# Performance work log

Hardware: AMD Instinct MI355X
Metric: run time of the kernel (lower is better)

The kernel has to match this reference:

```python
import jax, jax.numpy as jnp
import numpy as np

S, D, H, F = 8192, 2048, 2048, 8192
C_GATE = 8.0
EPS = 1e-6


def _rmsnorm(x, w, b):
    # eqx.nn.RMSNorm: x / sqrt(mean(x^2) + eps) * w + b, per row
    inv = jax.lax.rsqrt(jnp.mean(x * x, axis=-1, keepdims=True) + EPS)
    return x * inv * w + b


def _rglru(x, W_in, b_in, W_a, b_a, W_g, b_g, lam, W_out, b_out):
    # Real-Gated LRU (Griffin). x: [S, D] -> [S, D], hidden state size H.
    xh = x @ W_in.T + b_in                      # [S, H]
    r = jax.nn.sigmoid(x @ W_a.T + b_a)         # recurrence gate [S, H]
    g = jax.nn.sigmoid(x @ W_g.T + b_g)         # input gate      [S, H]
    log_a = C_GATE * r * jax.nn.log_sigmoid(lam)  # log a_t, a = sigmoid(lam)^(c*r)
    a = jnp.exp(log_a)                          # [S, H], in (0,1)
    b = jnp.sqrt(1.0 - jnp.exp(2.0 * log_a)) * (g * xh)

    def combine(e1, e2):
        a1, b1 = e1
        a2, b2 = e2
        return (a1 * a2, a2 * b1 + b2)

    _, h = jax.lax.associative_scan(combine, (a, b), axis=0)  # h_t = a_t h_{t-1} + b_t
    return h @ W_out.T + b_out                  # [S, D]


def _ffn(x, w1, b1, w2, b2):
    return jax.nn.gelu(x @ w1.T + b1) @ w2.T + b2


def setup_inputs() -> dict:
    key = jax.random.key(0)
    ks = jax.random.split(key, 16)
    s = 0.02  # weight init scale
    return {
        "x": jax.random.normal(ks[0], (S, D), jnp.float32),
        "W_in": jax.random.normal(ks[1], (H, D), jnp.float32) * s,
        "b_in": jnp.zeros((H,), jnp.float32),
        "W_a": jax.random.normal(ks[2], (H, D), jnp.float32) * s,
        "b_a": jnp.zeros((H,), jnp.float32),
        "W_g": jax.random.normal(ks[3], (H, D), jnp.float32) * s,
        "b_g": jnp.zeros((H,), jnp.float32),
        "lam": jax.random.normal(ks[4], (H,), jnp.float32),
        "W_out": jax.random.normal(ks[5], (D, H), jnp.float32) * s,
        "b_out": jnp.zeros((D,), jnp.float32),
        "ffn_w1": jax.random.normal(ks[6], (F, D), jnp.float32) * s,
        "ffn_b1": jnp.zeros((F,), jnp.float32),
        "ffn_w2": jax.random.normal(ks[7], (D, F), jnp.float32) * s,
        "ffn_b2": jnp.zeros((D,), jnp.float32),
        "act1_w": jax.random.normal(ks[8], (1, D), jnp.float32) * s,
        "act1_b": jnp.zeros((1,), jnp.float32),
        "act2_w": jax.random.normal(ks[9], (1, D), jnp.float32) * s,
        "act2_b": jnp.zeros((1,), jnp.float32),
        "norm1_w": jnp.ones((D,), jnp.float32),
        "norm1_b": jnp.zeros((D,), jnp.float32),
        "norm2_w": jnp.ones((D,), jnp.float32),
        "norm2_b": jnp.zeros((D,), jnp.float32),
        "u1": jax.random.uniform(ks[10], (S, 1), jnp.float32),
        "u2": jax.random.uniform(ks[11], (S, 1), jnp.float32),
    }


def reference(x, W_in, b_in, W_a, b_a, W_g, b_g, lam, W_out, b_out,
              ffn_w1, ffn_b1, ffn_w2, ffn_b2,
              act1_w, act1_b, act2_w, act2_b,
              norm1_w, norm1_b, norm2_w, norm2_b, u1, u2):
    # --- RG-LRU branch (dropout p=0 -> identity) ---
    residual = _rglru(x, W_in, b_in, W_a, b_a, W_g, b_g, lam, W_out, b_out)
    act_prob = jax.nn.sigmoid(residual @ act1_w.T + act1_b)  # [S, 1]
    act = u1 < act_prob                                      # stochastic gate
    residual = jnp.where(act, residual, 0.0)
    x = _rmsnorm(x + residual, norm1_w, norm1_b)
    # --- FFN branch ---
    residual = _ffn(x, ffn_w1, ffn_b1, ffn_w2, ffn_b2)
    act_prob = jax.nn.sigmoid(residual @ act2_w.T + act2_b)
    act = u2 < act_prob
    residual = jnp.where(act, residual, 0.0)
    x = _rmsnorm(x + residual, norm2_w, norm2_b)
    return x
```

## Files before the change

### kernel.cpp

```cpp
#include <hip/hip_runtime.h>

#define LDSW 40
#define SCAN_P 128
#define SCAN_L 64

typedef short short8 __attribute__((ext_vector_type(8)));
typedef float floatx4 __attribute__((ext_vector_type(4)));
typedef unsigned short u16;

__device__ __forceinline__ u16 bf16_rne(float v) {
    unsigned int u = __float_as_uint(v);
    u = u + 0x7fffu + ((u >> 16) & 1u);
    return (u16)(u >> 16);
}
__device__ __forceinline__ float bf16_to_f(u16 h) {
    return __uint_as_float(((unsigned int)h) << 16);
}
__device__ __forceinline__ float sigm(float x) { return 1.f / (1.f + expf(-x)); }
__device__ __forceinline__ float logsig(float x) {
    const float l = log1pf(expf(-fabsf(x)));
    return x >= 0.f ? -l : x - l;
}

__device__ __forceinline__ void cvt8(const float* p, short8& h8, short8& l8) {
    const float4 a = *(const float4*)p;
    const float4 b = *(const float4*)(p + 4);
    const float v[8] = {a.x, a.y, a.z, a.w, b.x, b.y, b.z, b.w};
#pragma unroll
    for (int j = 0; j < 8; ++j) {
        const u16 hh = bf16_rne(v[j]);
        h8[j] = (short)hh;
        l8[j] = (short)bf16_rne(v[j] - bf16_to_f(hh));
    }
}
__device__ __forceinline__ void cvt8h(const float* p, short8& h8) {
    const float4 a = *(const float4*)p;
    const float4 b = *(const float4*)(p + 4);
    const float v[8] = {a.x, a.y, a.z, a.w, b.x, b.y, b.z, b.w};
#pragma unroll
    for (int j = 0; j < 8; ++j) h8[j] = (short)bf16_rne(v[j]);
}

__device__ __forceinline__ void gld16(const u16* g, u16* l) {
    __builtin_amdgcn_global_load_lds(
        (const __attribute__((address_space(1))) void*)g,
        (__attribute__((address_space(3))) void*)l, 16, 0, 0);
}

template <int AFMT, int NPROD, int EPI, int ACC, int ST>
__global__ __launch_bounds__(256, 2) void gemm_f32(
    const float* __restrict__ Af, const u16* __restrict__ Au,
    const float* __restrict__ Bf, const float* __restrict__ bias,
    float* C, u16* Chi, u16* Clo, const float* Q,
    long ldA, long ldB, long ldC, int K)
{
    __shared__ __align__(16) u16 sAh[128 * LDSW];
    __shared__ __align__(16) u16 sBh[128 * LDSW];
    __shared__ __align__(16) u16 sAl[NPROD == 3 ? 128 * LDSW : 8];
    __shared__ __align__(16) u16 sBl[NPROD == 3 ? 128 * LDSW : 8];

    const int tid  = threadIdx.x;
    const int lane = tid & 63;
    const int wid  = tid >> 6;
    const int wm   = (wid >> 1) << 6;
    const int wn   = (wid & 1) << 6;
    const int m16  = lane & 15;
    const int kq   = lane >> 4;
    const int koff = kq << 3;
    const long bM  = (long)blockIdx.y << 7;
    const long bN  = (long)blockIdx.x << 7;
    const int sr   = tid >> 2;
    const int sc   = (tid & 3) << 3;

    floatx4 acc[4][4] = {};

#pragma unroll 1
    for (int k0 = 0; k0 < K; k0 += 32) {
        __syncthreads();
#pragma unroll
        for (int i = 0; i < 2; ++i) {
            const int r  = sr + (i << 6);
            const int ls = r * LDSW + sc;
            if constexpr (AFMT == 0) {
                if constexpr (NPROD == 3) {
                    short8 h8, l8;
                    cvt8(Af + (bM + r) * ldA + k0 + sc, h8, l8);
                    *(short8*)&sAh[ls] = h8;
                    *(short8*)&sAl[ls] = l8;
                } else {
                    short8 h8;
                    cvt8h(Af + (bM + r) * ldA + k0 + sc, h8);
                    *(short8*)&sAh[ls] = h8;
                }
            } else {
                *(short8*)&sAh[ls] = *(const short8*)(Au + (bM + r) * ldA + k0 + sc);
            }
            if constexpr (NPROD == 3) {
                short8 h8, l8;
                cvt8(Bf + (bN + r) * ldB + k0 + sc, h8, l8);
                *(short8*)&sBh[ls] = h8;
                *(short8*)&sBl[ls] = l8;
            } else {
                short8 h8;
                cvt8h(Bf + (bN + r) * ldB + k0 + sc, h8);
                *(short8*)&sBh[ls] = h8;
            }
        }
        __syncthreads();

        short8 ah[4], bh[4];
#pragma unroll
        for (int t = 0; t < 4; ++t) {
            ah[t] = *(const short8*)&sAh[(wm + t * 16 + m16) * LDSW + koff];
            bh[t] = *(const short8*)&sBh[(wn + t * 16 + m16) * LDSW + koff];
        }
#pragma unroll
        for (int mi = 0; mi < 4; ++mi)
#pragma unroll
            for (int ni = 0; ni < 4; ++ni)
                acc[mi][ni] = __builtin_amdgcn_mfma_f32_16x16x32_bf16(ah[mi], bh[ni], acc[mi][ni], 0, 0, 0);

        if constexpr (NPROD == 3) {
            short8 al[4], bl[4];
#pragma unroll
            for (int t = 0; t < 4; ++t) {
                al[t] = *(const short8*)&sAl[(wm + t * 16 + m16) * LDSW + koff];
                bl[t] = *(const short8*)&sBl[(wn + t * 16 + m16) * LDSW + koff];
            }
#pragma unroll
            for (int mi = 0; mi < 4; ++mi)
#pragma unroll
                for (int ni = 0; ni < 4; ++ni)
                    acc[mi][ni] = __builtin_amdgcn_mfma_f32_16x16x32_bf16(ah[mi], bl[ni], acc[mi][ni], 0, 0, 0);
#pragma unroll
            for (int mi = 0; mi < 4; ++mi)
#pragma unroll
                for (int ni = 0; ni < 4; ++ni)
                    acc[mi][ni] = __builtin_amdgcn_mfma_f32_16x16x32_bf16(al[mi], bh[ni], acc[mi][ni], 0, 0, 0);
        }
    }

    float bv[4];
#pragma unroll
    for (int ni = 0; ni < 4; ++ni) bv[ni] = bias ? bias[bN + wn + ni * 16 + m16] : 0.f;

#pragma unroll
    for (int mi = 0; mi < 4; ++mi) {
#pragma unroll
        for (int ni = 0; ni < 4; ++ni) {
#pragma unroll
            for (int r = 0; r < 4; ++r) {
                const long grow = bM + wm + mi * 16 + (kq << 2) + r;
                const long gcol = bN + wn + ni * 16 + m16;
                const long idx  = grow * ldC + gcol;
                float v = acc[mi][ni][r] + bv[ni];
                if constexpr (ACC) v += C[idx];
                if constexpr (EPI == 1) v *= Q[idx];
                if constexpr (EPI == 2)
                    v = 0.5f * v * (1.f + tanhf(0.7978845608028654f * (v + 0.044715f * v * v * v)));
                if constexpr (ST == 1) {
                    const u16 h = bf16_rne(v);
                    Chi[idx] = h;
                    Clo[idx] = bf16_rne(v - bf16_to_f(h));
                } else {
                    C[idx] = v;
                }
            }
        }
    }
}

template <int NPROD, int BFMT, int EPI, int ACC, int ST, int DOT>
__global__ __launch_bounds__(256, 2) void gemm_sp(
    const u16* __restrict__ Ah, const u16* __restrict__ Al,
    const u16* __restrict__ Bh, const u16* __restrict__ Bl,
    const float* __restrict__ Bf, const float* __restrict__ bias,
    float* C, u16* Chi, const float* Q,
    const float* __restrict__ vvec, float* dacc,
    long ldA, long ldB, long ldC, int K)
{
    __shared__ __align__(16) u16 sAh[128 * 32];
    __shared__ __align__(16) u16 sBh[128 * 32];
    __shared__ __align__(16) u16 sAl[NPROD == 3 ? 128 * 32 : 8];
    __shared__ __align__(16) u16 sBl[NPROD == 3 ? 128 * 32 : 8];

    const int tid  = threadIdx.x;
    const int lane = tid & 63;
    const int wid  = tid >> 6;
    const int wm   = (wid >> 1) << 6;
    const int wn   = (wid & 1) << 6;
    const int m16  = lane & 15;
    const int kq   = lane >> 4;
    const long bM  = (long)blockIdx.y << 7;
    const long bN  = (long)blockIdx.x << 7;

    const int  drow = (wid << 5) + (lane >> 2);
    const int  qsrc = (((lane & 3) ^ ((lane >> 3) & 3)) << 3);
    const long a0   = (bM + drow) * ldA + qsrc;
    const long a1   = a0 + 16 * ldA;
    const long b0   = (bN + drow) * ldB + qsrc;
    const long b1   = b0 + 16 * ldB;
    u16* const lA0  = &sAh[(wid << 5) << 5];
    u16* const lA1  = lA0 + 512;
    u16* const lB0  = &sBh[(wid << 5) << 5];
    u16* const lB1  = lB0 + 512;
    u16* const lAl0 = &sAl[NPROD == 3 ? ((wid << 5) << 5) : 0];
    u16* const lAl1 = lAl0 + (NPROD == 3 ? 512 : 0);
    u16* const lBl0 = &sBl[NPROD == 3 ? ((wid << 5) << 5) : 0];
    u16* const lBl1 = lBl0 + (NPROD == 3 ? 512 : 0);

    const int sr  = tid >> 2;
    const int sc  = (tid & 3) << 3;
    const int wch = (((tid & 3) ^ ((sr >> 1) & 3)) << 3);

    const int kr = ((kq ^ ((m16 >> 1) & 3)) << 3);

    floatx4 acc[4][4] = {};

#pragma unroll 1
    for (int k0 = 0; k0 < K; k0 += 32) {
        __syncthreads();
        gld16(Ah + a0 + k0, lA0);
        gld16(Ah + a1 + k0, lA1);
        if constexpr (NPROD == 3) {
            gld16(Al + a0 + k0, lAl0);
            gld16(Al + a1 + k0, lAl1);
        }
        if constexpr (BFMT == 1) {
            gld16(Bh + b0 + k0, lB0);
            gld16(Bh + b1 + k0, lB1);
            if constexpr (NPROD == 3) {
                gld16(Bl + b0 + k0, lBl0);
                gld16(Bl + b1 + k0, lBl1);
            }
        } else {
#pragma unroll
            for (int i = 0; i < 2; ++i) {
                const int r = sr + (i << 6);
                short8 h8, l8;
                cvt8(Bf + (bN + r) * ldB + k0 + sc, h8, l8);
                *(short8*)&sBh[(r << 5) + wch] = h8;
                *(short8*)&sBl[(r << 5) + wch] = l8;
            }
        }
        __syncthreads();

        short8 ah[4], bh[4];
#pragma unroll
        for (int t = 0; t < 4; ++t) {
            ah[t] = *(const short8*)&sAh[((wm + t * 16 + m16) << 5) + kr];
            bh[t] = *(const short8*)&sBh[((wn + t * 16 + m16) << 5) + kr];
        }
#pragma unroll
        for (int mi = 0; mi < 4; ++mi)
#pragma unroll
            for (int ni = 0; ni < 4; ++ni)
                acc[mi][ni] = __builtin_amdgcn_mfma_f32_16x16x32_bf16(ah[mi], bh[ni], acc[mi][ni], 0, 0, 0);

        if constexpr (NPROD == 3) {
            short8 al[4], bl[4];
#pragma unroll
            for (int t = 0; t < 4; ++t) {
                al[t] = *(const short8*)&sAl[((wm + t * 16 + m16) << 5) + kr];
                bl[t] = *(const short8*)&sBl[((wn + t * 16 + m16) << 5) + kr];
            }
#pragma unroll
            for (int mi = 0; mi < 4; ++mi)
#pragma unroll
                for (int ni = 0; ni < 4; ++ni)
                    acc[mi][ni] = __builtin_amdgcn_mfma_f32_16x16x32_bf16(ah[mi], bl[ni], acc[mi][ni], 0, 0, 0);
#pragma unroll
            for (int mi = 0; mi < 4; ++mi)
#pragma unroll
                for (int ni = 0; ni < 4; ++ni)
                    acc[mi][ni] = __builtin_amdgcn_mfma_f32_16x16x32_bf16(al[mi], bh[ni], acc[mi][ni], 0, 0, 0);
        }
    }

    float bv[4];
#pragma unroll
    for (int ni = 0; ni < 4; ++ni) bv[ni] = bias ? bias[bN + wn + ni * 16 + m16] : 0.f;
    float vv[4] = {}, ls[4] = {};
    if constexpr (EPI == 3 || DOT == 1) {
#pragma unroll
        for (int ni = 0; ni < 4; ++ni) {
            vv[ni] = vvec[bN + wn + ni * 16 + m16];
            if constexpr (EPI == 3) ls[ni] = logsig(vv[ni]);
        }
    }
    float ds[4][4] = {};

#pragma unroll
    for (int mi = 0; mi < 4; ++mi) {
#pragma unroll
        for (int ni = 0; ni < 4; ++ni) {
#pragma unroll
            for (int r = 0; r < 4; ++r) {
                const long grow = bM + wm + mi * 16 + (kq << 2) + r;
                const long gcol = bN + wn + ni * 16 + m16;
                const long idx  = grow * ldC + gcol;
                float v = acc[mi][ni][r] + bv[ni];
                if constexpr (EPI == 1) v *= Q[idx];
                if constexpr (EPI == 2)
                    v = 0.5f * v * (1.f + tanhf(0.7978845608028654f * (v + 0.044715f * v * v * v)));
                if constexpr (EPI == 3) v = expf(8.f * sigm(v) * ls[ni]);
                if constexpr (EPI == 4) {
                    const float a = Q[idx];
                    v = sqrtf(fmaxf(1.f - a * a, 0.f)) * sigm(v);
                }
                if constexpr (ACC) v += C[idx];
                if constexpr (DOT) ds[mi][r] += v * vv[ni];
                if constexpr (ST == 1) Chi[idx] = bf16_rne(v);
                else C[idx] = v;
            }
        }
    }

    if constexpr (DOT) {
#pragma unroll
        for (int mi = 0; mi < 4; ++mi)
#pragma unroll
            for (int r = 0; r < 4; ++r) {
                float s = ds[mi][r];
                s += __shfl_xor(s, 1);
                s += __shfl_xor(s, 2);
                s += __shfl_xor(s, 4);
                s += __shfl_xor(s, 8);
                if (m16 == 0)
                    atomicAdd(&dacc[bM + wm + mi * 16 + (kq << 2) + r], s);
            }
    }
}

template <int HASLO>
__global__ __launch_bounds__(256) void split_kernel(
    const float* __restrict__ src, long lds,
    u16* __restrict__ hi, u16* __restrict__ lo, long ldd)
{
    const long r = blockIdx.x;
    const int  c = threadIdx.x << 3;
    const float* p = src + r * lds + c;
    const float4 a = *(const float4*)p;
    const float4 b = *(const float4*)(p + 4);
    const float v[8] = {a.x, a.y, a.z, a.w, b.x, b.y, b.z, b.w};
    short8 h8, l8;
#pragma unroll
    for (int j = 0; j < 8; ++j) {
        const u16 hh = bf16_rne(v[j]);
        h8[j] = (short)hh;
        if constexpr (HASLO) l8[j] = (short)bf16_rne(v[j] - bf16_to_f(hh));
    }
    *(short8*)&hi[r * ldd + c] = h8;
    if constexpr (HASLO) *(short8*)&lo[r * ldd + c] = l8;
}

__global__ __launch_bounds__(256) void zb2init_kernel(
    float* __restrict__ zb2, const float* __restrict__ zc2)
{
    zb2[blockIdx.x * 256 + threadIdx.x] = zc2[0];
}

__global__ __launch_bounds__(256) void aq_kernel(
    float* za, float* zg, const float* __restrict__ lam)
{
    const long i = ((long)blockIdx.x * 256 + threadIdx.x) * 4;
    const int  c = (int)(i & 2047);
    const float4 zav = *(const float4*)(za + i);
    const float4 zgv = *(const float4*)(zg + i);
    const float4 lmv = *(const float4*)(lam + c);
    float4 av, qv;
    const float zaa[4] = {zav.x, zav.y, zav.z, zav.w};
    const float zga[4] = {zgv.x, zgv.y, zgv.z, zgv.w};
    const float lma[4] = {lmv.x, lmv.y, lmv.z, lmv.w};
    float aa[4], qa[4];
#pragma unroll
    for (int j = 0; j < 4; ++j) {
        const float r  = sigm(zaa[j]);
        const float g  = sigm(zga[j]);
        const float la = 8.f * r * logsig(lma[j]);
        aa[j] = expf(la);
        qa[j] = sqrtf(fmaxf(1.f - expf(2.f * la), 0.f)) * g;
    }
    av.x = aa[0]; av.y = aa[1]; av.z = aa[2]; av.w = aa[3];
    qv.x = qa[0]; qv.y = qa[1]; qv.z = qa[2]; qv.w = qa[3];
    *(float4*)(za + i) = av;
    *(float4*)(zg + i) = qv;
}

__global__ __launch_bounds__(256) void scan_partial(
    const float* __restrict__ A, const float* __restrict__ B,
    float* __restrict__ Aagg, float* __restrict__ Bagg)
{
    const int c = blockIdx.x * 256 + threadIdx.x;
    const int p = blockIdx.y;
    const long base = (long)p * SCAN_L * 2048 + c;
    float Ar = 1.f, Br = 0.f;
    for (int t = 0; t < SCAN_L; ++t) {
        const float at = A[base + (long)t * 2048];
        const float bt = B[base + (long)t * 2048];
        Ar *= at;
        Br = Br * at + bt;
    }
    Aagg[p * 2048 + c] = Ar;
    Bagg[p * 2048 + c] = Br;
}

__global__ __launch_bounds__(256) void scan_combine(
    const float* __restrict__ Aagg, const float* __restrict__ Bagg,
    float* __restrict__ Hini)
{
    const int c = blockIdx.x * 256 + threadIdx.x;
    float h = 0.f;
    for (int p = 0; p < SCAN_P; ++p) {
        Hini[p * 2048 + c] = h;
        h = Aagg[p * 2048 + c] * h + Bagg[p * 2048 + c];
    }
}

__global__ __launch_bounds__(256) void scan_final(
    float* A, const float* __restrict__ B, const float* __restrict__ Hini)
{
    const int c = blockIdx.x * 256 + threadIdx.x;
    const int p = blockIdx.y;
    const long base = (long)p * SCAN_L * 2048 + c;
    float h = Hini[p * 2048 + c];
    for (int t = 0; t < SCAN_L; ++t) {
        const long idx = base + (long)t * 2048;
        h = A[idx] * h + B[idx];
        A[idx] = h;
    }
}

__global__ __launch_bounds__(256) void vpart_kernel(
    const float* __restrict__ W, const float* __restrict__ w,
    float* __restrict__ part, long ldW, int dchunk)
{
    const int j  = blockIdx.x * 256 + threadIdx.x;
    const int d0 = blockIdx.y * dchunk;
    float s = 0.f;
    for (int d = 0; d < dchunk; ++d) s += W[(long)(d0 + d) * ldW + j] * w[d0 + d];
    part[(long)blockIdx.y * ldW + j] = s;
}

__global__ __launch_bounds__(256) void vreduce_kernel(
    const float* __restrict__ part, float* __restrict__ v, long ldW, int nch)
{
    const int j = blockIdx.x * 256 + threadIdx.x;
    float s = 0.f;
    for (int c = 0; c < nch; ++c) s += part[(long)c * ldW + j];
    v[j] = s;
}

__global__ __launch_bounds__(256) void dotc_kernel(
    const float* __restrict__ a, const float* __restrict__ b,
    const float* __restrict__ bias1, float* __restrict__ out)
{
    __shared__ float red[4];
    const int tid = threadIdx.x, lane = tid & 63, wid = tid >> 6;
    float s = 0.f;
    for (int d = tid; d < 2048; d += 256) s += a[d] * b[d];
#pragma unroll
    for (int off = 32; off > 0; off >>= 1) s += __shfl_down(s, off);
    if (lane == 0) red[wid] = s;
    __syncthreads();
    if (tid == 0) out[0] = red[0] + red[1] + red[2] + red[3] + bias1[0];
}

template <int INIT>
__global__ __launch_bounds__(256) void zacc_kernel(
    const u16* __restrict__ uHi, const u16* __restrict__ uLo,
    const float* __restrict__ v2s, const float* __restrict__ zc,
    float* __restrict__ zb, int L)
{
    __shared__ float red[4];
    const int tid = threadIdx.x, lane = tid & 63, wid = tid >> 6;
    const long s = blockIdx.x;
    const long base = s * (long)L;
    float dot = 0.f;
    for (int f = tid; f < L; f += 256)
        dot += (bf16_to_f(uHi[base + f]) + bf16_to_f(uLo[base + f])) * v2s[f];
#pragma unroll
    for (int off = 32; off > 0; off >>= 1) dot += __shfl_down(dot, off);
    if (lane == 0) red[wid] = dot;
    __syncthreads();
    if (tid == 0) {
        const float t = red[0] + red[1] + red[2] + red[3];
        zb[s] = INIT ? (zc[0] + t) : (zb[s] + t);
    }
}

__global__ __launch_bounds__(256) void gate1_kernel(
    const float* __restrict__ x, float* res1x1,
    const float* __restrict__ h,
    const float* __restrict__ v1, const float* __restrict__ zc1,
    const float* __restrict__ u1,
    const float* __restrict__ nw, const float* __restrict__ nb)
{
    __shared__ float red[4];
    const int tid = threadIdx.x, lane = tid & 63, wid = tid >> 6;
    const long s = blockIdx.x;
    const long base = s * 2048;

    float dot = 0.f;
#pragma unroll
    for (int k = 0; k < 8; ++k) {
        const int d = tid + (k << 8);
        dot += h[base + d] * v1[d];
    }
#pragma unroll
    for (int off = 32; off > 0; off >>= 1) dot += __shfl_down(dot, off);
    if (lane == 0) red[wid] = dot;
    __syncthreads();
    const float z = red[0] + red[1] + red[2] + red[3] + zc1[0];
    __syncthreads();

    const float g = (u1[s] < sigm(z)) ? 1.f : 0.f;

    float yv[8];
    float ss = 0.f;
#pragma unroll
    for (int k = 0; k < 8; ++k) {
        const int d = tid + (k << 8);
        const float y = x[base + d] + g * res1x1[base + d];
        yv[k] = y;
        ss += y * y;
    }
#pragma unroll
    for (int off = 32; off > 0; off >>= 1) ss += __shfl_down(ss, off);
    if (lane == 0) red[wid] = ss;
    __syncthreads();
    const float inv = rsqrtf((red[0] + red[1] + red[2] + red[3]) * (1.f / 2048.f) + 1e-6f);

#pragma unroll
    for (int k = 0; k < 8; ++k) {
        const int d = tid + (k << 8);
        res1x1[base + d] = yv[k] * inv * nw[d] + nb[d];
    }
}

__global__ __launch_bounds__(256) void gate1s_kernel(
    const float* __restrict__ x, float* res1x1,
    const float* __restrict__ h,
    const float* __restrict__ v1, const float* __restrict__ zc1,
    const float* __restrict__ u1,
    const float* __restrict__ nw, const float* __restrict__ nb)
{
    __shared__ float red[4];
    const int tid = threadIdx.x, lane = tid & 63, wid = tid >> 6;
    const long s = blockIdx.x;
    const long base = s * 2048;

    float dot = 0.f;
#pragma unroll
    for (int k = 0; k < 8; ++k) {
        const int d = tid + (k << 8);
        dot += h[base + d] * v1[d];
    }
#pragma unroll
    for (int off = 32; off > 0; off >>= 1) dot += __shfl_down(dot, off);
    if (lane == 0) red[wid] = dot;
    __syncthreads();
    const float z = red[0] + red[1] + red[2] + red[3] + zc1[0];
    __syncthreads();

    const float g = (u1[s] < sigm(z)) ? 1.f : 0.f;

    float yv[8];
    float ss = 0.f;
#pragma unroll
    for (int k = 0; k < 8; ++k) {
        const int d = tid + (k << 8);
        const float y = x[base + d] + g * res1x1[base + d];
        yv[k] = y;
        ss += y * y;
    }
#pragma unroll
    for (int off = 32; off > 0; off >>= 1) ss += __shfl_down(ss, off);
    if (lane == 0) red[wid] = ss;
    __syncthreads();
    const float inv = rsqrtf((red[0] + red[1] + red[2] + red[3]) * (1.f / 2048.f) + 1e-6f);

    u16* xs = (u16*)res1x1;
    const long sb = s * 4096;
#pragma unroll
    for (int k = 0; k < 8; ++k) {
        const int d = tid + (k << 8);
        const float o = yv[k] * inv * nw[d] + nb[d];
        const u16 hh = bf16_rne(o);
        xs[sb + d] = hh;
        xs[sb + 2048 + d] = bf16_rne(o - bf16_to_f(hh));
    }
}

__global__ __launch_bounds__(256) void gate2_kernel(
    float* x1out, const float* __restrict__ res2,
    const float* __restrict__ zb2, const float* __restrict__ u2,
    const float* __restrict__ nw, const float* __restrict__ nb)
{
    __shared__ float red[4];
    const int tid = threadIdx.x, lane = tid & 63, wid = tid >> 6;
    const long s = blockIdx.x;
    const long base = s * 2048;

    const float g = (u2[s] < sigm(zb2[s])) ? 1.f : 0.f;

    float yv[8];
    float ss = 0.f;
#pragma unroll
    for (int k = 0; k < 8; ++k) {
        const int d = tid + (k << 8);
        const float y = x1out[base + d] + g * res2[base + d];
        yv[k] = y;
        ss += y * y;
    }
#pragma unroll
    for (int off = 32; off > 0; off >>= 1) ss += __shfl_down(ss, off);
    if (lane == 0) red[wid] = ss;
    __syncthreads();
    const float inv = rsqrtf((red[0] + red[1] + red[2] + red[3]) * (1.f / 2048.f) + 1e-6f);

#pragma unroll
    for (int k = 0; k < 8; ++k) {
        const int d = tid + (k << 8);
        x1out[base + d] = yv[k] * inv * nw[d] + nb[d];
    }
}

__global__ __launch_bounds__(256) void gate2s_kernel(
    float* x1out, const float* __restrict__ res2,
    const float* __restrict__ zb2, const float* __restrict__ u2,
    const float* __restrict__ nw, const float* __restrict__ nb)
{
    __shared__ float red[4];
    const int tid = threadIdx.x, lane = tid & 63, wid = tid >> 6;
    const long s = blockIdx.x;
    const long base = s * 2048;
    const u16* xs = (const u16*)x1out;
    const long sb = s * 4096;

    const float g = (u2[s] < sigm(zb2[s])) ? 1.f : 0.f;

    float yv[8];
    float ss = 0.f;
#pragma unroll
    for (int k = 0; k < 8; ++k) {
        const int d = tid + (k << 8);
        const float x1 = bf16_to_f(xs[sb + d]) + bf16_to_f(xs[sb + 2048 + d]);
        const float y = x1 + g * res2[base + d];
        yv[k] = y;
        ss += y * y;
    }
#pragma unroll
    for (int off = 32; off > 0; off >>= 1) ss += __shfl_down(ss, off);
    if (lane == 0) red[wid] = ss;
    __syncthreads();
    const float inv = rsqrtf((red[0] + red[1] + red[2] + red[3]) * (1.f / 2048.f) + 1e-6f);

#pragma unroll
    for (int k = 0; k < 8; ++k) {
        const int d = tid + (k << 8);
        x1out[base + d] = yv[k] * inv * nw[d] + nb[d];
    }
}

extern "C" void kernel_launch(void* const* d_in, const int* in_sizes, int n_in,
                              void* d_out, int out_size, void* d_ws, size_t ws_size,
                              hipStream_t stream)
{
    const float* x     = (const float*)d_in[0];
    const float* W_in  = (const float*)d_in[1];
    const float* b_in  = (const float*)d_in[2];
    const float* W_a   = (const float*)d_in[3];
    const float* b_a   = (const float*)d_in[4];
    const float* W_g   = (const float*)d_in[5];
    const float* b_g   = (const float*)d_in[6];
    const float* lam   = (const float*)d_in[7];
    const float* W_out = (const float*)d_in[8];
    const float* b_out = (const float*)d_in[9];
    const float* w1    = (const float*)d_in[10];
    const float* fb1   = (const float*)d_in[11];
    const float* w2    = (const float*)d_in[12];
    const float* fb2   = (const float*)d_in[13];
    const float* a1w   = (const float*)d_in[14];
    const float* a1b   = (const float*)d_in[15];
    const float* a2w   = (const float*)d_in[16];
    const float* a2b   = (const float*)d_in[17];
    const float* n1w   = (const float*)d_in[18];
    const float* n1b   = (const float*)d_in[19];
    const float* n2w   = (const float*)d_in[20];
    const float* n2b   = (const float*)d_in[21];
    const float* u1    = (const float*)d_in[22];
    const float* u2    = (const float*)d_in[23];
    (void)in_sizes; (void)n_in; (void)out_size;

    float* dob = (float*)d_out;

    char* ws = (char*)d_ws;
    size_t o = 0;
    auto take = [&](size_t bytes) -> char* {
        char* p = ws + o;
        o += (bytes + 255) & ~(size_t)255;
        return p;
    };

    float* Aagg = (float*)take((size_t)SCAN_P * 2048 * 4);
    float* Bagg = (float*)take((size_t)SCAN_P * 2048 * 4);
    float* Hini = (float*)take((size_t)SCAN_P * 2048 * 4);
    float* v1   = (float*)take(2048 * 4);
    float* v2   = (float*)take(8192 * 4);
    float* vp   = (float*)take(16 * 8192 * 4);
    float* zc1  = (float*)take(256);
    float* zc2  = (float*)take(256);
    float* zb2  = (float*)take(8192 * 4);

    float* slabA = (float*)take(64ull << 20);
    const bool pathA = ws_size >= o + (64ull << 20);
    float* slabB = nullptr;
    float* res2b = nullptr;
    if (pathA) slabB = (float*)take(64ull << 20);
    else       res2b = (float*)take(16ull << 20);
    if (o > ws_size) return;

    const dim3 blk(256);

    vpart_kernel<<<dim3(8, 16), blk, 0, stream>>>(W_out, a1w, vp, 2048, 128);
    vreduce_kernel<<<8, blk, 0, stream>>>(vp, v1, 2048, 16);
    vpart_kernel<<<dim3(32, 16), blk, 0, stream>>>(w2, a2w, vp, 8192, 128);
    vreduce_kernel<<<32, blk, 0, stream>>>(vp, v2, 8192, 16);
    dotc_kernel<<<1, blk, 0, stream>>>(b_out, a1w, a1b, zc1);
    dotc_kernel<<<1, blk, 0, stream>>>(fb2, a2w, a2b, zc2);

    if (pathA) {
        u16* const xh = (u16*)slabA;
        u16* const xl = xh + (1u << 24);
        split_kernel<1><<<8192, blk, 0, stream>>>(x, 2048, xh, xl, 2048);

        gemm_sp<3, 0, 3, 0, 0, 0><<<dim3(16, 64), blk, 0, stream>>>(
            xh, xl, nullptr, nullptr, W_a, b_a, slabB, nullptr, nullptr, lam, nullptr,
            2048, 2048, 2048, 2048);
        gemm_sp<3, 0, 4, 0, 0, 0><<<dim3(16, 64), blk, 0, stream>>>(
            xh, xl, nullptr, nullptr, W_g, b_g, dob, nullptr, slabB, nullptr, nullptr,
            2048, 2048, 2048, 2048);
        gemm_sp<3, 0, 1, 0, 0, 0><<<dim3(16, 64), blk, 0, stream>>>(
            xh, xl, nullptr, nullptr, W_in, b_in, dob, nullptr, dob, nullptr, nullptr,
            2048, 2048, 2048, 2048);

        scan_partial<<<dim3(8, SCAN_P), blk, 0, stream>>>(slabB, dob, Aagg, Bagg);
        scan_combine<<<8, blk, 0, stream>>>(Aagg, Bagg, Hini);
        scan_final<<<dim3(8, SCAN_P), blk, 0, stream>>>(slabB, dob, Hini);

        u16* const hH  = (u16*)slabA;
        u16* const woH = hH + (1u << 24);
        split_kernel<0><<<8192, blk, 0, stream>>>(slabB, 2048, hH, nullptr, 2048);
        split_kernel<0><<<2048, blk, 0, stream>>>(W_out, 2048, woH, nullptr, 2048);
        gemm_sp<1, 1, 0, 0, 0, 0><<<dim3(16, 64), blk, 0, stream>>>(
            hH, nullptr, woH, nullptr, nullptr, b_out, dob, nullptr, nullptr, nullptr, nullptr,
            2048, 2048, 2048, 2048);

        gate1s_kernel<<<8192, blk, 0, stream>>>(x, dob, slabB, v1, zc1, u1, n1w, n1b);

        zb2init_kernel<<<32, blk, 0, stream>>>(zb2, zc2);

        u16* const uH  = (u16*)slabA;
        u16* const w1H = uH + (1u << 24);
        u16* const w1L = w1H + (1u << 22);
        u16* const w2H = w1H + (1u << 23);
        u16* const x1h = (u16*)dob;
        for (int c = 0; c < 4; ++c) {
            const long f0 = (long)c << 11;
            split_kernel<1><<<2048, blk, 0, stream>>>(w1 + f0 * 2048, 2048, w1H, w1L, 2048);
            split_kernel<0><<<2048, blk, 0, stream>>>(w2 + f0, 8192, w2H, nullptr, 2048);
            gemm_sp<3, 1, 2, 0, 1, 1><<<dim3(16, 64), blk, 0, stream>>>(
                x1h, x1h + 2048, w1H, w1L, nullptr, fb1 + f0, nullptr, uH, nullptr,
                v2 + f0, zb2, 4096, 2048, 2048, 2048);
            if (c == 0)
                gemm_sp<1, 1, 0, 0, 0, 0><<<dim3(16, 64), blk, 0, stream>>>(
                    uH, nullptr, w2H, nullptr, nullptr, fb2, slabB, nullptr, nullptr,
                    nullptr, nullptr, 2048, 2048, 2048, 2048);
            else
                gemm_sp<1, 1, 0, 1, 0, 0><<<dim3(16, 64), blk, 0, stream>>>(
                    uH, nullptr, w2H, nullptr, nullptr, nullptr, slabB, nullptr, nullptr,
                    nullptr, nullptr, 2048, 2048, 2048, 2048);
        }
        gate2s_kernel<<<8192, blk, 0, stream>>>(dob, slabB, zb2, u2, n2w, n2b);
    } else {
        u16* uHi = (u16*)slabA;
        u16* uLo = uHi + (1u << 24);

        gemm_f32<0, 3, 0, 0, 0><<<dim3(16, 64), blk, 0, stream>>>(
            x, nullptr, W_a, b_a, slabA, nullptr, nullptr, nullptr, 2048, 2048, 2048, 2048);
        gemm_f32<0, 3, 0, 0, 0><<<dim3(16, 64), blk, 0, stream>>>(
            x, nullptr, W_g, b_g, dob, nullptr, nullptr, nullptr, 2048, 2048, 2048, 2048);
        aq_kernel<<<16384, blk, 0, stream>>>(slabA, dob, lam);
        gemm_f32<0, 3, 1, 0, 0><<<dim3(16, 64), blk, 0, stream>>>(
            x, nullptr, W_in, b_in, dob, nullptr, nullptr, dob, 2048, 2048, 2048, 2048);
        scan_partial<<<dim3(8, SCAN_P), blk, 0, stream>>>(slabA, dob, Aagg, Bagg);
        scan_combine<<<8, blk, 0, stream>>>(Aagg, Bagg, Hini);
        scan_final<<<dim3(8, SCAN_P), blk, 0, stream>>>(slabA, dob, Hini);
        gemm_f32<0, 1, 0, 0, 0><<<dim3(16, 64), blk, 0, stream>>>(
            slabA, nullptr, W_out, b_out, dob, nullptr, nullptr, nullptr, 2048, 2048, 2048, 2048);
        gate1_kernel<<<8192, blk, 0, stream>>>(x, dob, slabA, v1, zc1, u1, n1w, n1b);
        for (int rb = 0; rb < 4; ++rb) {
            const long roff = (long)rb * 2048;
            gemm_f32<0, 3, 2, 0, 1><<<dim3(64, 16), blk, 0, stream>>>(
                dob + roff * 2048, nullptr, w1, fb1,
                nullptr, uHi, uLo, nullptr, 2048, 2048, 8192, 2048);
            zacc_kernel<1><<<2048, blk, 0, stream>>>(uHi, uLo, v2, zc2, zb2 + roff, 8192);
            gemm_f32<1, 1, 0, 0, 0><<<dim3(16, 16), blk, 0, stream>>>(
                nullptr, uHi, w2, fb2, res2b, nullptr, nullptr, nullptr,
                8192, 8192, 2048, 8192);
            gate2_kernel<<<2048, blk, 0, stream>>>(
                dob + roff * 2048, res2b, zb2 + roff, u2 + roff, n2w, n2b);
        }
    }
}
```

Baseline: 2.686 ms.

## Add 256x256-tile 512-thread bf16 MFMA GEMM and fuse h bf16 split into scan

Introduces gemm8, a 512-thread kernel computing 256x256 output tiles. It double-buffers global-to-LDS loads with explicit vmcnt waits, uses XOR-swizzled LDS reads, and raises wave priority around the MFMA blocks. This kernel replaces gemm_sp for the W_out projection and the FFN w1 and w2 GEMMs. Separately, scan_final now writes the bf16 copy of h directly, which removes one split_kernel pass over the 8192x2048 hidden state. Larger tiles cut global traffic per FLOP, but they raise register and LDS pressure and halve the number of blocks, which could hurt occupancy and load balance.

```diff
diff --git a/kernel.cpp b/kernel.cpp
--- a/kernel.cpp
+++ b/kernel.cpp
@@ -46,6 +46,12 @@
         (const __attribute__((address_space(1))) void*)g,
         (__attribute__((address_space(3))) void*)l, 16, 0, 0);
 }
+
+__device__ __forceinline__ void vmwait8() { asm volatile("s_waitcnt vmcnt(8)" ::: "memory"); }
+__device__ __forceinline__ void vmwait4() { asm volatile("s_waitcnt vmcnt(4)" ::: "memory"); }
+__device__ __forceinline__ void vmwait0() { asm volatile("s_waitcnt vmcnt(0)" ::: "memory"); }
+__device__ __forceinline__ void lgwait0() { asm volatile("s_waitcnt lgkmcnt(0)" ::: "memory"); }
+__device__ __forceinline__ void barr()    { asm volatile("s_barrier" ::: "memory"); }
 
 template <int AFMT, int NPROD, int EPI, int ACC, int ST>
 __global__ __launch_bounds__(256, 2) void gemm_f32(
@@ -332,6 +338,195 @@
     }
 }
 
+template <int NPROD, int EPI, int ACC, int ST, int DOT>
+__global__ __launch_bounds__(512, 2) void gemm8(
+    const u16* __restrict__ Ah, const u16* __restrict__ Al,
+    const u16* __restrict__ Bh, const u16* __restrict__ Bl,
+    const float* __restrict__ bias,
+    float* C, u16* Chi,
+    const float* __restrict__ vvec, float* dacc,
+    long ldA, long ldB, long ldC, int K)
+{
+    constexpr int NPL = (NPROD == 3) ? 4 : 2;
+    __shared__ __align__(16) u16 lds[2][NPL][8192];
+
+    const int tid  = threadIdx.x;
+    const int lane = tid & 63;
+    const int wid  = tid >> 6;
+    const int wr   = wid >> 2;
+    const int wc   = wid & 3;
+    const int m16  = lane & 15;
+    const int kq   = lane >> 4;
+    const long bM  = (long)blockIdx.y << 8;
+    const long bN  = (long)blockIdx.x << 8;
+
+    const int  drow = (wid << 5) + (lane >> 2);
+    const int  qsrc = (((lane & 3) ^ ((lane >> 3) & 3)) << 3);
+    const u16* gA0  = Ah + (bM + drow) * ldA + qsrc;
+    const u16* gA1  = gA0 + (ldA << 4);
+    const u16* gB0  = Bh + (bN + drow) * ldB + qsrc;
+    const u16* gB1  = gB0 + (ldB << 4);
+    const u16* gAl0 = (NPROD == 3 ? Al : Ah) + (bM + drow) * ldA + qsrc;
+    const u16* gAl1 = gAl0 + (ldA << 4);
+    const u16* gBl0 = (NPROD == 3 ? Bl : Bh) + (bN + drow) * ldB + qsrc;
+    const u16* gBl1 = gBl0 + (ldB << 4);
+
+    const int lwb = wid << 10;
+    const int kr  = ((kq ^ ((m16 >> 1) & 3)) << 3);
+
+    const int NT = K >> 5;
+
+    auto stage = [&](int buf, int t) {
+        const long k0 = (long)t << 5;
+        gld16(gA0 + k0, &lds[buf][0][lwb]);
+        gld16(gA1 + k0, &lds[buf][0][lwb + 512]);
+        gld16(gB0 + k0, &lds[buf][1][lwb]);
+        gld16(gB1 + k0, &lds[buf][1][lwb + 512]);
+        if constexpr (NPROD == 3) {
+            gld16(gAl0 + k0, &lds[buf][2][lwb]);
+            gld16(gAl1 + k0, &lds[buf][2][lwb + 512]);
+            gld16(gBl0 + k0, &lds[buf][3][lwb]);
+            gld16(gBl1 + k0, &lds[buf][3][lwb + 512]);
+        }
+    };
+
+    floatx4 acc[8][4] = {};
+    short8 bh[4], bl[4];
+
+    stage(0, 0);
+    stage(1, 1);
+    if constexpr (NPROD == 3) vmwait8(); else vmwait4();
+    barr();
+
+    const int arow = (wr << 7) + m16;
+    const int brow = (wc << 6) + m16;
+
+#pragma unroll 1
+    for (int t = 0; t < NT; ++t) {
+        const int p = t & 1;
+#pragma unroll
+        for (int q = 0; q < 4; ++q) {
+            const int r0 = arow + (q << 5);
+            const int r1 = r0 + 16;
+            short8 ah0 = *(const short8*)&lds[p][0][(r0 << 5) + kr];
+            short8 ah1 = *(const short8*)&lds[p][0][(r1 << 5) + kr];
+            short8 al0 = {}, al1 = {};
+            if constexpr (NPROD == 3) {
+                al0 = *(const short8*)&lds[p][2][(r0 << 5) + kr];
+                al1 = *(const short8*)&lds[p][2][(r1 << 5) + kr];
+            }
+            if (q == 0) {
+#pragma unroll
+                for (int ni = 0; ni < 4; ++ni) {
+                    const int rb = (brow + (ni << 4)) << 5;
+                    bh[ni] = *(const short8*)&lds[p][1][rb + kr];
+                    if constexpr (NPROD == 3)
+                        bl[ni] = *(const short8*)&lds[p][3][rb + kr];
+                }
+            }
+            if (q < 3) {
+                lgwait0();
+                __builtin_amdgcn_sched_barrier(0);
+                __builtin_amdgcn_s_setprio(1);
+#pragma unroll
+                for (int ni = 0; ni < 4; ++ni) {
+                    acc[2 * q][ni]     = __builtin_amdgcn_mfma_f32_16x16x32_bf16(ah0, bh[ni], acc[2 * q][ni], 0, 0, 0);
+                    acc[2 * q + 1][ni] = __builtin_amdgcn_mfma_f32_16x16x32_bf16(ah1, bh[ni], acc[2 * q + 1][ni], 0, 0, 0);
+                }
+                if constexpr (NPROD == 3) {
+#pragma unroll
+                    for (int ni = 0; ni < 4; ++ni) {
+                        acc[2 * q][ni]     = __builtin_amdgcn_mfma_f32_16x16x32_bf16(ah0, bl[ni], acc[2 * q][ni], 0, 0, 0);
+                        acc[2 * q + 1][ni] = __builtin_amdgcn_mfma_f32_16x16x32_bf16(ah1, bl[ni], acc[2 * q + 1][ni], 0, 0, 0);
+                    }
+#pragma unroll
+                    for (int ni = 0; ni < 4; ++ni) {
+                        acc[2 * q][ni]     = __builtin_amdgcn_mfma_f32_16x16x32_bf16(al0, bh[ni], acc[2 * q][ni], 0, 0, 0);
+                        acc[2 * q + 1][ni] = __builtin_amdgcn_mfma_f32_16x16x32_bf16(al1, bh[ni], acc[2 * q + 1][ni], 0, 0, 0);
+                    }
+                }
+                __builtin_amdgcn_s_setprio(0);
+                barr();
+            } else {
+                lgwait0();
+                barr();
+                const bool pf = (t + 2 < NT);
+                if (pf) stage(p, t + 2);
+                __builtin_amdgcn_s_setprio(1);
+#pragma unroll
+                for (int ni = 0; ni < 4; ++ni) {
+                    acc[6][ni] = __builtin_amdgcn_mfma_f32_16x16x32_bf16(ah0, bh[ni], acc[6][ni], 0, 0, 0);
+                    acc[7][ni] = __builtin_amdgcn_mfma_f32_16x16x32_bf16(ah1, bh[ni], acc[7][ni], 0, 0, 0);
+                }
+                if constexpr (NPROD == 3) {
+#pragma unroll
+                    for (int ni = 0; ni < 4; ++ni) {
+                        acc[6][ni] = __builtin_amdgcn_mfma_f32_16x16x32_bf16(ah0, bl[ni], acc[6][ni], 0, 0, 0);
+                        acc[7][ni] = __builtin_amdgcn_mfma_f32_16x16x32_bf16(ah1, bl[ni], acc[7][ni], 0, 0, 0);
+                    }
+#pragma unroll
+                    for (int ni = 0; ni < 4; ++ni) {
+                        acc[6][ni] = __builtin_amdgcn_mfma_f32_16x16x32_bf16(al0, bh[ni], acc[6][ni], 0, 0, 0);
+                        acc[7][ni] = __builtin_amdgcn_mfma_f32_16x16x32_bf16(al1, bh[ni], acc[7][ni], 0, 0, 0);
+                    }
+                }
+                __builtin_amdgcn_s_setprio(0);
+                if (pf) {
+                    if constexpr (NPROD == 3) vmwait8(); else vmwait4();
+                } else {
+                    vmwait0();
+                }
+                barr();
+            }
+        }
+    }
+
+    float bv[4];
+#pragma unroll
+    for (int ni = 0; ni < 4; ++ni) bv[ni] = bias ? bias[bN + (wc << 6) + (ni << 4) + m16] : 0.f;
+    float vv[4] = {};
+    if constexpr (DOT) {
+#pragma unroll
+        for (int ni = 0; ni < 4; ++ni) vv[ni] = vvec[bN + (wc << 6) + (ni << 4) + m16];
+    }
+    float ds[8][4] = {};
+
+#pragma unroll
+    for (int mi = 0; mi < 8; ++mi) {
+#pragma unroll
+        for (int ni = 0; ni < 4; ++ni) {
+#pragma unroll
+            for (int r = 0; r < 4; ++r) {
+                const long grow = bM + (wr << 7) + (mi << 4) + (kq << 2) + r;
+                const long gcol = bN + (wc << 6) + (ni << 4) + m16;
+                const long idx  = grow * ldC + gcol;
+                float v = acc[mi][ni][r] + bv[ni];
+                if constexpr (EPI == 2)
+                    v = 0.5f * v * (1.f + tanhf(0.7978845608028654f * (v + 0.044715f * v * v * v)));
+                if constexpr (ACC) v += C[idx];
+                if constexpr (DOT) ds[mi][r] += v * vv[ni];
+                if constexpr (ST == 1) Chi[idx] = bf16_rne(v);
+                else C[idx] = v;
+            }
+        }
+    }
+
+    if constexpr (DOT) {
+#pragma unroll
+        for (int mi = 0; mi < 8; ++mi)
+#pragma unroll
+            for (int r = 0; r < 4; ++r) {
+                float s = ds[mi][r];
+                s += __shfl_xor(s, 1);
+                s += __shfl_xor(s, 2);
+                s += __shfl_xor(s, 4);
+                s += __shfl_xor(s, 8);
+                if (m16 == 0)
+                    atomicAdd(&dacc[bM + (wr << 7) + (mi << 4) + (kq << 2) + r], s);
+            }
+    }
+}
+
 template <int HASLO>
 __global__ __launch_bounds__(256) void split_kernel(
     const float* __restrict__ src, long lds,
@@ -418,7 +613,8 @@
 }
 
 __global__ __launch_bounds__(256) void scan_final(
-    float* A, const float* __restrict__ B, const float* __restrict__ Hini)
+    float* A, const float* __restrict__ B, const float* __restrict__ Hini,
+    u16* __restrict__ Hhi)
 {
     const int c = blockIdx.x * 256 + threadIdx.x;
     const int p = blockIdx.y;
@@ -428,6 +624,7 @@
         const long idx = base + (long)t * 2048;
         h = A[idx] * h + B[idx];
         A[idx] = h;
+        if (Hhi) Hhi[idx] = bf16_rne(h);
     }
 }
 
@@ -745,16 +942,15 @@
             xh, xl, nullptr, nullptr, W_in, b_in, dob, nullptr, dob, nullptr, nullptr,
             2048, 2048, 2048, 2048);
 
+        u16* const hH = (u16*)slabA;
         scan_partial<<<dim3(8, SCAN_P), blk, 0, stream>>>(slabB, dob, Aagg, Bagg);
         scan_combine<<<8, blk, 0, stream>>>(Aagg, Bagg, Hini);
-        scan_final<<<dim3(8, SCAN_P), blk, 0, stream>>>(slabB, dob, Hini);
-
-        u16* const hH  = (u16*)slabA;
+        scan_final<<<dim3(8, SCAN_P), blk, 0, stream>>>(slabB, dob, Hini, hH);
+
         u16* const woH = hH + (1u << 24);
-        split_kernel<0><<<8192, blk, 0, stream>>>(slabB, 2048, hH, nullptr, 2048);
         split_kernel<0><<<2048, blk, 0, stream>>>(W_out, 2048, woH, nullptr, 2048);
-        gemm_sp<1, 1, 0, 0, 0, 0><<<dim3(16, 64), blk, 0, stream>>>(
-            hH, nullptr, woH, nullptr, nullptr, b_out, dob, nullptr, nullptr, nullptr, nullptr,
+        gemm8<1, 0, 0, 0, 0><<<dim3(8, 32), dim3(512), 0, stream>>>(
+            hH, nullptr, woH, nullptr, b_out, dob, nullptr, nullptr, nullptr,
             2048, 2048, 2048, 2048);
 
         gate1s_kernel<<<8192, blk, 0, stream>>>(x, dob, slabB, v1, zc1, u1, n1w, n1b);
@@ -770,17 +966,17 @@
             const long f0 = (long)c << 11;
             split_kernel<1><<<2048, blk, 0, stream>>>(w1 + f0 * 2048, 2048, w1H, w1L, 2048);
             split_kernel<0><<<2048, blk, 0, stream>>>(w2 + f0, 8192, w2H, nullptr, 2048);
-            gemm_sp<3, 1, 2, 0, 1, 1><<<dim3(16, 64), blk, 0, stream>>>(
-                x1h, x1h + 2048, w1H, w1L, nullptr, fb1 + f0, nullptr, uH, nullptr,
+            gemm8<3, 2, 0, 1, 1><<<dim3(8, 32), dim3(512), 0, stream>>>(
+                x1h, x1h + 2048, w1H, w1L, fb1 + f0, nullptr, uH,
                 v2 + f0, zb2, 4096, 2048, 2048, 2048);
             if (c == 0)
-                gemm_sp<1, 1, 0, 0, 0, 0><<<dim3(16, 64), blk, 0, stream>>>(
-                    uH, nullptr, w2H, nullptr, nullptr, fb2, slabB, nullptr, nullptr,
-                    nullptr, nullptr, 2048, 2048, 2048, 2048);
+                gemm8<1, 0, 0, 0, 0><<<dim3(8, 32), dim3(512), 0, stream>>>(
+                    uH, nullptr, w2H, nullptr, fb2, slabB, nullptr, nullptr, nullptr,
+                    2048, 2048, 2048, 2048);
             else
-                gemm_sp<1, 1, 0, 1, 0, 0><<<dim3(16, 64), blk, 0, stream>>>(
-                    uH, nullptr, w2H, nullptr, nullptr, nullptr, slabB, nullptr, nullptr,
-                    nullptr, nullptr, 2048, 2048, 2048, 2048);
+                gemm8<1, 0, 1, 0, 0><<<dim3(8, 32), dim3(512), 0, stream>>>(
+                    uH, nullptr, w2H, nullptr, nullptr, slabB, nullptr, nullptr, nullptr,
+                    2048, 2048, 2048, 2048);
         }
         gate2s_kernel<<<8192, blk, 0, stream>>>(dob, slabB, zb2, u2, n2w, n2b);
     } else {
@@ -796,7 +992,7 @@
             x, nullptr, W_in, b_in, dob, nullptr, nullptr, dob, 2048, 2048, 2048, 2048);
         scan_partial<<<dim3(8, SCAN_P), blk, 0, stream>>>(slabA, dob, Aagg, Bagg);
         scan_combine<<<8, blk, 0, stream>>>(Aagg, Bagg, Hini);
-        scan_final<<<dim3(8, SCAN_P), blk, 0, stream>>>(slabA, dob, Hini);
+        scan_final<<<dim3(8, SCAN_P), blk, 0, stream>>>(slabA, dob, Hini, nullptr);
         gemm_f32<0, 1, 0, 0, 0><<<dim3(16, 64), blk, 0, stream>>>(
             slabA, nullptr, W_out, b_out, dob, nullptr, nullptr, nullptr, 2048, 2048, 2048, 2048);
         gate1_kernel<<<8192, blk, 0, stream>>>(x, dob, slabA, v1, zc1, u1, n1w, n1b);
```

Result: no change. 2.680 ms (-0.2%).
